# Optimization experiments

Measured on AMD Instinct MI355X. Metric: run time of the kernel, lower is better.

## Reference

```python
import jax, jax.numpy as jnp
import numpy as np

ALPHA = 0.5
BETA = 0.5


def _attend(qk, feat, W, wp, b):
    """One additive co-attention stage.
    qk:   (B, K)     projected query
    feat: (B, N, D)  keys/values
    W:    (D, K), wp: (2K, 1), b: (N,)
    returns (B, D) attention-weighted sum of feat.
    """
    proj = jnp.einsum('bnd,dk->bnk', feat, W)                    # (B,N,K)
    q = jnp.broadcast_to(qk[:, None, :], proj.shape)             # repeat query
    H = jnp.tanh(jnp.concatenate([q, proj], axis=-1))            # (B,N,2K)
    logits = jnp.einsum('bnk,k->bn', H, wp[:, 0]) + b            # (B,N)
    P = jax.nn.softmax(logits, axis=-1)
    return jnp.einsum('bn,bnd->bd', P, feat)                     # (B,D)


def setup_inputs() -> dict:
    key = jax.random.key(0)
    B, R, S, G, E, D, K = 256, 49, 128, 20, 30, 1024, 256
    ks = jax.random.split(key, 19)
    w = lambda k, shp: 0.05 * jax.random.normal(k, shp, jnp.float32)
    return {
        'ifeature_h': jax.random.normal(ks[0], (B, R, D), jnp.float32),
        'tfeature_h': jax.random.normal(ks[1], (B, S, D), jnp.float32),
        'cfeature':   jax.random.normal(ks[2], (B, G, D), jnp.float32),
        'efeature':   jax.random.normal(ks[3], (B, E, D), jnp.float32),
        'w_Vit_0':  w(ks[4],  (D, K)),
        'w_Vc_0':   w(ks[5],  (D, K)),
        'w_Pc_0':   w(ks[6],  (2 * K, 1)),
        'b_Pc_0':   jnp.zeros((G,), jnp.float32),
        'w_Ve_0':   w(ks[7],  (D, K)),
        'w_Pe_0':   w(ks[8],  (2 * K, 1)),
        'b_Pe_0':   jnp.zeros((E,), jnp.float32),
        'w_Vi_1':   w(ks[9],  (D, K)),
        'w_Vtce_1': w(ks[10], (D, K)),
        'w_Pi_1':   w(ks[11], (2 * K, 1)),
        'b_Pi_1':   jnp.zeros((R,), jnp.float32),
        'w_Vice_2': w(ks[12], (D, K)),
        'w_Vt_2':   w(ks[13], (D, K)),
        'w_Pt_2':   w(ks[14], (2 * K, 1)),
        'b_Pt_2':   jnp.zeros((S,), jnp.float32),
    }


def reference(ifeature_h, tfeature_h, cfeature, efeature,
              w_Vit_0, w_Vc_0, w_Pc_0, b_Pc_0,
              w_Ve_0, w_Pe_0, b_Pe_0,
              w_Vi_1, w_Vtce_1, w_Pi_1, b_Pi_1,
              w_Vice_2, w_Vt_2, w_Pt_2, b_Pt_2):
    ifeat = jnp.mean(ifeature_h, axis=1)   # (B, D)
    tfeat = jnp.mean(tfeature_h, axis=1)   # (B, D)

    # stage 0: image+text query attends over caption group and title
    q0 = (ifeat + tfeat) @ w_Vit_0                               # (B, K)
    Vc = _attend(q0, cfeature, w_Vc_0, w_Pc_0, b_Pc_0)           # (B, D)
    Ve = _attend(q0, efeature, w_Ve_0, w_Pe_0, b_Pe_0)           # (B, D)

    # stage 1: text+caption+title query attends over image regions
    q1 = (tfeat + ALPHA * Vc + BETA * Ve) @ w_Vtce_1
    Vi = _attend(q1, ifeature_h, w_Vi_1, w_Pi_1, b_Pi_1)

    # stage 2: image+caption+title query attends over text tokens
    q2 = (Vi + ALPHA * Vc + BETA * Ve) @ w_Vice_2
    Vt = _attend(q2, tfeature_h, w_Vt_2, w_Pt_2, b_Pt_2)

    return Vi + Vt + ALPHA * Vc + BETA * Ve
```

## Files before the change

### kernel.cpp

```cpp
#include <hip/hip_runtime.h>
#include <hip/hip_bf16.h>
#include <stdint.h>


#define D_DIM 1024
#define K_OUT 256
#define BM 64
#define BK 64
#define NT 16

typedef float f32x4 __attribute__((ext_vector_type(4)));
typedef short bf16x8 __attribute__((ext_vector_type(8)));
typedef unsigned short u16x8 __attribute__((ext_vector_type(8)));

static __device__ __forceinline__ unsigned short f2bf(float f) {
    return __builtin_bit_cast(unsigned short, __float2bfloat16(f));
}

static __device__ __forceinline__ float fast_tanh(float x) {
    float e = __expf(2.0f * x);
    return 1.0f - 2.0f / (e + 1.0f);
}

__global__ __launch_bounds__(256) void convert_wt(
    const float* __restrict__ w_c, const float* __restrict__ w_e,
    const float* __restrict__ w_i, const float* __restrict__ w_t,
    unsigned short* __restrict__ wtf)
{
    const float* wsel[4] = {w_c, w_e, w_i, w_t};
    const float* W = wsel[blockIdx.x];
    unsigned short* out = wtf + (size_t)blockIdx.x * (K_OUT * D_DIM);
    const int kb = blockIdx.y;
    const int t = threadIdx.x;

    unsigned short tmp[16];
#pragma unroll
    for (int j = 0; j < 16; ++j)
        tmp[j] = f2bf(W[(size_t)(kb * 16 + j) * K_OUT + t]);

    u16x8 lo, hi;
#pragma unroll
    for (int j = 0; j < 8; ++j) { lo[j] = tmp[j]; hi[j] = tmp[8 + j]; }
    unsigned short* dst = out + (size_t)kb * 4096 + t * 16;
    *reinterpret_cast<u16x8*>(dst) = lo;
    *reinterpret_cast<u16x8*>(dst + 8) = hi;
}

struct GemmStage {
    const float* feat;
    const unsigned short* wt;
    const float* wp;
    float* s_out;
    int blk_start;
};

__global__ __launch_bounds__(256, 3) void logits_gemm(
    GemmStage g0, GemmStage g1, GemmStage g2, GemmStage g3)
{
    __shared__ __align__(16) unsigned char As[2][BM * 128];
    __shared__ float partial[BM][4];

    const int bid = blockIdx.x;
    GemmStage st;
    if (bid < g1.blk_start) st = g0;
    else if (bid < g2.blk_start) st = g1;
    else if (bid < g3.blk_start) st = g2;
    else st = g3;
    const int m0 = (bid - st.blk_start) * BM;

    const int t = threadIdx.x;
    const int r = t >> 2, qd = t & 3;
    const int wv = t >> 6, lane = t & 63;
    const int q = lane >> 4, c16 = lane & 15;

    const float* aptr = st.feat + (size_t)(m0 + r) * D_DIM + qd * 16;
    const int wo0 = r * 128 + (((qd * 2    ) ^ (r & 7)) << 4);
    const int wo1 = r * 128 + (((qd * 2 + 1) ^ (r & 7)) << 4);
    const unsigned short* bb = st.wt + (q >> 1) * 4096
                             + ((wv * 64 + c16) << 4) + (q & 1) * 8;
    const int ck0 = ((0 * 4 + q) ^ (c16 & 7)) << 4;
    const int ck1 = ((1 * 4 + q) ^ (c16 & 7)) << 4;

    float wpf[4];
#pragma unroll
    for (int nt = 0; nt < 4; ++nt) wpf[nt] = st.wp[K_OUT + wv * 64 + nt * 16 + c16];

    f32x4 acc[4][4];
#pragma unroll
    for (int i = 0; i < 4; ++i)
#pragma unroll
        for (int j = 0; j < 4; ++j) acc[i][j] = (f32x4){0.f, 0.f, 0.f, 0.f};

    f32x4 pa[4];
#pragma unroll
    for (int j = 0; j < 4; ++j)
        pa[j] = *reinterpret_cast<const f32x4*>(aptr + j * 4);
    {
        u16x8 o0, o1;
#pragma unroll
        for (int j = 0; j < 4; ++j) {
            o0[j] = f2bf(pa[0][j]); o0[4 + j] = f2bf(pa[1][j]);
            o1[j] = f2bf(pa[2][j]); o1[4 + j] = f2bf(pa[3][j]);
        }
        *reinterpret_cast<u16x8*>(&As[0][wo0]) = o0;
        *reinterpret_cast<u16x8*>(&As[0][wo1]) = o1;
    }

#pragma unroll 1
    for (int kt = 0; kt < NT; ++kt) {
        __syncthreads();
        u16x8 bfr[2][4];
        const unsigned short* bk = bb + kt * 16384;
#pragma unroll
        for (int ks = 0; ks < 2; ++ks)
#pragma unroll
            for (int nt = 0; nt < 4; ++nt)
                bfr[ks][nt] = *reinterpret_cast<const u16x8*>(bk + ks * 8192 + nt * 256);
        const int ktn = (kt + 1) & 15;
#pragma unroll
        for (int j = 0; j < 4; ++j)
            pa[j] = *reinterpret_cast<const f32x4*>(aptr + ktn * 64 + j * 4);
        const unsigned char* buf = As[kt & 1];
#pragma unroll
        for (int ks = 0; ks < 2; ++ks) {
            const int ck = ks ? ck1 : ck0;
            bf16x8 af[4];
#pragma unroll
            for (int mt = 0; mt < 4; ++mt)
                af[mt] = *reinterpret_cast<const bf16x8*>(&buf[(mt * 16 + c16) * 128 + ck]);
#pragma unroll
            for (int mt = 0; mt < 4; ++mt)
#pragma unroll
                for (int nt = 0; nt < 4; ++nt)
                    acc[mt][nt] = __builtin_amdgcn_mfma_f32_16x16x32_bf16(
                        af[mt], __builtin_bit_cast(bf16x8, bfr[ks][nt]),
                        acc[mt][nt], 0, 0, 0);
        }
        if (kt + 1 < NT) {
            u16x8 o0, o1;
#pragma unroll
            for (int j = 0; j < 4; ++j) {
                o0[j] = f2bf(pa[0][j]); o0[4 + j] = f2bf(pa[1][j]);
                o1[j] = f2bf(pa[2][j]); o1[4 + j] = f2bf(pa[3][j]);
            }
            unsigned char* nbuf = As[(kt + 1) & 1];
            *reinterpret_cast<u16x8*>(&nbuf[wo0]) = o0;
            *reinterpret_cast<u16x8*>(&nbuf[wo1]) = o1;
        }
    }

#pragma unroll
    for (int mt = 0; mt < 4; ++mt) {
#pragma unroll
        for (int rg = 0; rg < 4; ++rg) {
            float v = 0.f;
#pragma unroll
            for (int nt = 0; nt < 4; ++nt)
                v += fast_tanh(acc[mt][nt][rg]) * wpf[nt];
            v += __shfl_xor(v, 1);
            v += __shfl_xor(v, 2);
            v += __shfl_xor(v, 4);
            v += __shfl_xor(v, 8);
            if (c16 == 0) partial[mt * 16 + q * 4 + rg][wv] = v;
        }
    }
    __syncthreads();
    if (t < BM)
        st.s_out[m0 + t] = partial[t][0] + partial[t][1] + partial[t][2] + partial[t][3];
}

struct PVStage {
    const float* s;
    const float* bias;
    const float* feat;
    float* v_out;
    int N;
};

__global__ __launch_bounds__(256) void softmax_pv(
    PVStage p0, PVStage p1, PVStage p2, PVStage p3)
{
    PVStage st = (blockIdx.y == 0) ? p0 : (blockIdx.y == 1) ? p1
               : (blockIdx.y == 2) ? p2 : p3;
    const int b = blockIdx.x, t = threadIdx.x;
    const int N = st.N;

    __shared__ float P[128];
    __shared__ float inv_s;

    if (t < N) P[t] = st.s[b * N + t] + st.bias[t];
    __syncthreads();
    if (t < 64) {
        float m = -3.4e38f;
        for (int n = t; n < N; n += 64) m = fmaxf(m, P[n]);
#pragma unroll
        for (int sh = 32; sh; sh >>= 1) m = fmaxf(m, __shfl_xor(m, sh));
        float ssum = 0.f;
        for (int n = t; n < N; n += 64) { float e = __expf(P[n] - m); P[n] = e; ssum += e; }
#pragma unroll
        for (int sh = 32; sh; sh >>= 1) ssum += __shfl_xor(ssum, sh);
        if (t == 0) inv_s = 1.0f / ssum;
    }
    __syncthreads();
    const float inv = inv_s;

    f32x4 accv = (f32x4){0.f, 0.f, 0.f, 0.f};
    const float* fb = st.feat + (size_t)b * N * D_DIM + t * 4;
    for (int n = 0; n < N; ++n) {
        f32x4 f = *reinterpret_cast<const f32x4*>(fb + (size_t)n * D_DIM);
        accv += (P[n] * inv) * f;
    }
    *reinterpret_cast<f32x4*>(&st.v_out[(size_t)b * D_DIM + t * 4]) = accv;
}

__global__ __launch_bounds__(256) void combine_out(
    const float* __restrict__ vc, const float* __restrict__ ve,
    const float* __restrict__ vi, const float* __restrict__ vt,
    float* __restrict__ out)
{
    const int i = (blockIdx.x * 256 + threadIdx.x) * 4;
    f32x4 a = *reinterpret_cast<const f32x4*>(vi + i);
    f32x4 bb = *reinterpret_cast<const f32x4*>(vt + i);
    f32x4 c = *reinterpret_cast<const f32x4*>(vc + i);
    f32x4 e = *reinterpret_cast<const f32x4*>(ve + i);
    *reinterpret_cast<f32x4*>(out + i) = a + bb + 0.5f * c + 0.5f * e;
}

extern "C" void kernel_launch(void* const* d_in, const int* in_sizes, int n_in,
                              void* d_out, int out_size, void* d_ws, size_t ws_size,
                              hipStream_t stream)
{
    const float* ifeature = (const float*)d_in[0];
    const float* tfeature = (const float*)d_in[1];
    const float* cfeature = (const float*)d_in[2];
    const float* efeature = (const float*)d_in[3];
    const float* w_Vc = (const float*)d_in[5];
    const float* w_Pc = (const float*)d_in[6];
    const float* b_Pc = (const float*)d_in[7];
    const float* w_Ve = (const float*)d_in[8];
    const float* w_Pe = (const float*)d_in[9];
    const float* b_Pe = (const float*)d_in[10];
    const float* w_Vi = (const float*)d_in[11];
    const float* w_Pi = (const float*)d_in[13];
    const float* b_Pi = (const float*)d_in[14];
    const float* w_Vt = (const float*)d_in[16];
    const float* w_Pt = (const float*)d_in[17];
    const float* b_Pt = (const float*)d_in[18];

    char* ws = (char*)d_ws;
    unsigned short* wtf = (unsigned short*)ws;
    float* s_c = (float*)(ws + 2u * 1024 * 1024);
    float* s_e = s_c + 5120;
    float* s_i = s_e + 7680;
    float* s_t = s_i + 12544;
    float* v_c = (float*)(ws + 3u * 1024 * 1024);
    float* v_e = v_c + 256 * 1024;
    float* v_i = v_e + 256 * 1024;
    float* v_t = v_i + 256 * 1024;

    convert_wt<<<dim3(4, 64), 256, 0, stream>>>(w_Vc, w_Ve, w_Vi, w_Vt, wtf);

    GemmStage g0{cfeature, wtf,          w_Pc, s_c, 0};
    GemmStage g1{efeature, wtf + 262144, w_Pe, s_e, 80};
    GemmStage g2{ifeature, wtf + 524288, w_Pi, s_i, 200};
    GemmStage g3{tfeature, wtf + 786432, w_Pt, s_t, 396};
    logits_gemm<<<908, 256, 0, stream>>>(g0, g1, g2, g3);

    PVStage p0{s_c, b_Pc, cfeature, v_c, 20};
    PVStage p1{s_e, b_Pe, efeature, v_e, 30};
    PVStage p2{s_i, b_Pi, ifeature, v_i, 49};
    PVStage p3{s_t, b_Pt, tfeature, v_t, 128};
    softmax_pv<<<dim3(256, 4), 256, 0, stream>>>(p0, p1, p2, p3);

    combine_out<<<256, 256, 0, stream>>>(v_c, v_e, v_i, v_t, (float*)d_out);
}
```

Baseline: 99.38 us.

## Use 512-thread blocks with deeper A-prefetch in logits GEMM

Doubles the logits GEMM block to 8 waves, each covering 32 output columns instead of 64, which halves per-thread accumulators and weight loads. The A-tile global loads are prefetched two k-steps ahead through two register sets in a manually unrolled loop, and each thread now converts and stores one 16-byte chunk per step. The goal is more memory-level parallelism and occupancy to hide the fp32 feature-load latency. In exchange it adds more barrier participants, and each A fragment is read from LDS by twice as many waves.

```diff
diff --git a/kernel.cpp b/kernel.cpp
--- a/kernel.cpp
+++ b/kernel.cpp
@@ -54,11 +54,11 @@
     int blk_start;
 };
 
-__global__ __launch_bounds__(256, 3) void logits_gemm(
+__global__ __launch_bounds__(512, 4) void logits_gemm(
     GemmStage g0, GemmStage g1, GemmStage g2, GemmStage g3)
 {
     __shared__ __align__(16) unsigned char As[2][BM * 128];
-    __shared__ float partial[BM][4];
+    __shared__ float partial[BM][8];
 
     const int bid = blockIdx.x;
     GemmStage st;
@@ -69,85 +69,97 @@
     const int m0 = (bid - st.blk_start) * BM;
 
     const int t = threadIdx.x;
-    const int r = t >> 2, qd = t & 3;
     const int wv = t >> 6, lane = t & 63;
     const int q = lane >> 4, c16 = lane & 15;
 
-    const float* aptr = st.feat + (size_t)(m0 + r) * D_DIM + qd * 16;
-    const int wo0 = r * 128 + (((qd * 2    ) ^ (r & 7)) << 4);
-    const int wo1 = r * 128 + (((qd * 2 + 1) ^ (r & 7)) << 4);
-    const unsigned short* bb = st.wt + (q >> 1) * 4096
-                             + ((wv * 64 + c16) << 4) + (q & 1) * 8;
-    const int ck0 = ((0 * 4 + q) ^ (c16 & 7)) << 4;
-    const int ck1 = ((1 * 4 + q) ^ (c16 & 7)) << 4;
-
-    float wpf[4];
-#pragma unroll
-    for (int nt = 0; nt < 4; ++nt) wpf[nt] = st.wp[K_OUT + wv * 64 + nt * 16 + c16];
-
-    f32x4 acc[4][4];
+    const int r = t >> 3, p = t & 7;
+    const int lc = p ^ (r & 7);
+    const float* aptr = st.feat + (size_t)(m0 + r) * D_DIM + lc * 8;
+    const int wofs = r * 128 + p * 16;
+
+    int rofs[4][2];
+#pragma unroll
+    for (int mt = 0; mt < 4; ++mt)
+#pragma unroll
+        for (int ks = 0; ks < 2; ++ks)
+            rofs[mt][ks] = (mt * 16 + c16) * 128 + ((((ks * 4 + q)) ^ (c16 & 7)) << 4);
+
+    const unsigned short* bb = st.wt + (size_t)(q >> 1) * 4096
+                             + ((wv * 32 + c16) << 4) + (q & 1) * 8;
+
+    float wpf[2];
+#pragma unroll
+    for (int nt = 0; nt < 2; ++nt) wpf[nt] = st.wp[K_OUT + wv * 32 + nt * 16 + c16];
+
+    f32x4 acc[4][2];
 #pragma unroll
     for (int i = 0; i < 4; ++i)
 #pragma unroll
-        for (int j = 0; j < 4; ++j) acc[i][j] = (f32x4){0.f, 0.f, 0.f, 0.f};
-
-    f32x4 pa[4];
-#pragma unroll
-    for (int j = 0; j < 4; ++j)
-        pa[j] = *reinterpret_cast<const f32x4*>(aptr + j * 4);
+        for (int j = 0; j < 2; ++j) acc[i][j] = (f32x4){0.f, 0.f, 0.f, 0.f};
+
+    f32x4 sa0, sa1, sb0, sb1;
+
+    sa0 = *reinterpret_cast<const f32x4*>(aptr);
+    sa1 = *reinterpret_cast<const f32x4*>(aptr + 4);
     {
-        u16x8 o0, o1;
-#pragma unroll
-        for (int j = 0; j < 4; ++j) {
-            o0[j] = f2bf(pa[0][j]); o0[4 + j] = f2bf(pa[1][j]);
-            o1[j] = f2bf(pa[2][j]); o1[4 + j] = f2bf(pa[3][j]);
-        }
-        *reinterpret_cast<u16x8*>(&As[0][wo0]) = o0;
-        *reinterpret_cast<u16x8*>(&As[0][wo1]) = o1;
+        u16x8 o;
+#pragma unroll
+        for (int j = 0; j < 4; ++j) { o[j] = f2bf(sa0[j]); o[4 + j] = f2bf(sa1[j]); }
+        *reinterpret_cast<u16x8*>(&As[0][wofs]) = o;
+    }
+    sa0 = *reinterpret_cast<const f32x4*>(aptr + 64);
+    sa1 = *reinterpret_cast<const f32x4*>(aptr + 68);
+    sb0 = *reinterpret_cast<const f32x4*>(aptr + 128);
+    sb1 = *reinterpret_cast<const f32x4*>(aptr + 132);
+    __syncthreads();
+
+#define GEMM_BODY(KT, BUFC, BUFN, S0, S1)                                      \
+    {                                                                          \
+        const int kt_ = (KT);                                                  \
+        u16x8 rb[2][2];                                                        \
+        const unsigned short* bk = bb + (size_t)kt_ * 16384;                   \
+        _Pragma("unroll")                                                      \
+        for (int ks = 0; ks < 2; ++ks)                                         \
+            _Pragma("unroll")                                                  \
+            for (int nt = 0; nt < 2; ++nt)                                     \
+                rb[ks][nt] = *reinterpret_cast<const u16x8*>(                  \
+                    bk + ks * 8192 + nt * 256);                                \
+        _Pragma("unroll")                                                      \
+        for (int ks = 0; ks < 2; ++ks) {                                       \
+            bf16x8 af[4];                                                      \
+            _Pragma("unroll")                                                  \
+            for (int mt = 0; mt < 4; ++mt)                                     \
+                af[mt] = *reinterpret_cast<const bf16x8*>(                     \
+                    &As[BUFC][rofs[mt][ks]]);                                  \
+            _Pragma("unroll")                                                  \
+            for (int mt = 0; mt < 4; ++mt)                                     \
+                _Pragma("unroll")                                              \
+                for (int nt = 0; nt < 2; ++nt)                                 \
+                    acc[mt][nt] = __builtin_amdgcn_mfma_f32_16x16x32_bf16(     \
+                        af[mt], __builtin_bit_cast(bf16x8, rb[ks][nt]),        \
+                        acc[mt][nt], 0, 0, 0);                                 \
+        }                                                                      \
+        if (kt_ + 1 < NT) {                                                    \
+            u16x8 o;                                                           \
+            _Pragma("unroll")                                                  \
+            for (int j = 0; j < 4; ++j) {                                      \
+                o[j] = f2bf(S0[j]); o[4 + j] = f2bf(S1[j]);                    \
+            }                                                                  \
+            *reinterpret_cast<u16x8*>(&As[BUFN][wofs]) = o;                    \
+            if (kt_ + 3 < NT) {                                                \
+                S0 = *reinterpret_cast<const f32x4*>(aptr + (kt_ + 3) * 64);   \
+                S1 = *reinterpret_cast<const f32x4*>(aptr + (kt_ + 3) * 64 + 4);\
+            }                                                                  \
+        }                                                                      \
+        __syncthreads();                                                       \
     }
 
 #pragma unroll 1
-    for (int kt = 0; kt < NT; ++kt) {
-        __syncthreads();
-        u16x8 bfr[2][4];
-        const unsigned short* bk = bb + kt * 16384;
-#pragma unroll
-        for (int ks = 0; ks < 2; ++ks)
-#pragma unroll
-            for (int nt = 0; nt < 4; ++nt)
-                bfr[ks][nt] = *reinterpret_cast<const u16x8*>(bk + ks * 8192 + nt * 256);
-        const int ktn = (kt + 1) & 15;
-#pragma unroll
-        for (int j = 0; j < 4; ++j)
-            pa[j] = *reinterpret_cast<const f32x4*>(aptr + ktn * 64 + j * 4);
-        const unsigned char* buf = As[kt & 1];
-#pragma unroll
-        for (int ks = 0; ks < 2; ++ks) {
-            const int ck = ks ? ck1 : ck0;
-            bf16x8 af[4];
-#pragma unroll
-            for (int mt = 0; mt < 4; ++mt)
-                af[mt] = *reinterpret_cast<const bf16x8*>(&buf[(mt * 16 + c16) * 128 + ck]);
-#pragma unroll
-            for (int mt = 0; mt < 4; ++mt)
-#pragma unroll
-                for (int nt = 0; nt < 4; ++nt)
-                    acc[mt][nt] = __builtin_amdgcn_mfma_f32_16x16x32_bf16(
-                        af[mt], __builtin_bit_cast(bf16x8, bfr[ks][nt]),
-                        acc[mt][nt], 0, 0, 0);
-        }
-        if (kt + 1 < NT) {
-            u16x8 o0, o1;
-#pragma unroll
-            for (int j = 0; j < 4; ++j) {
-                o0[j] = f2bf(pa[0][j]); o0[4 + j] = f2bf(pa[1][j]);
-                o1[j] = f2bf(pa[2][j]); o1[4 + j] = f2bf(pa[3][j]);
-            }
-            unsigned char* nbuf = As[(kt + 1) & 1];
-            *reinterpret_cast<u16x8*>(&nbuf[wo0]) = o0;
-            *reinterpret_cast<u16x8*>(&nbuf[wo1]) = o1;
-        }
-    }
+    for (int k2 = 0; k2 < NT; k2 += 2) {
+        GEMM_BODY(k2,     0, 1, sa0, sa1)
+        GEMM_BODY(k2 + 1, 1, 0, sb0, sb1)
+    }
+#undef GEMM_BODY
 
 #pragma unroll
     for (int mt = 0; mt < 4; ++mt) {
@@ -155,7 +167,7 @@
         for (int rg = 0; rg < 4; ++rg) {
             float v = 0.f;
 #pragma unroll
-            for (int nt = 0; nt < 4; ++nt)
+            for (int nt = 0; nt < 2; ++nt)
                 v += fast_tanh(acc[mt][nt][rg]) * wpf[nt];
             v += __shfl_xor(v, 1);
             v += __shfl_xor(v, 2);
@@ -165,8 +177,12 @@
         }
     }
     __syncthreads();
-    if (t < BM)
-        st.s_out[m0 + t] = partial[t][0] + partial[t][1] + partial[t][2] + partial[t][3];
+    if (t < BM) {
+        float v = 0.f;
+#pragma unroll
+        for (int w = 0; w < 8; ++w) v += partial[t][w];
+        st.s_out[m0 + t] = v;
+    }
 }
 
 struct PVStage {
@@ -264,7 +280,7 @@
     GemmStage g1{efeature, wtf + 262144, w_Pe, s_e, 80};
     GemmStage g2{ifeature, wtf + 524288, w_Pi, s_i, 200};
     GemmStage g3{tfeature, wtf + 786432, w_Pt, s_t, 396};
-    logits_gemm<<<908, 256, 0, stream>>>(g0, g1, g2, g3);
+    logits_gemm<<<908, 512, 0, stream>>>(g0, g1, g2, g3);
 
     PVStage p0{s_c, b_Pc, cfeature, v_c, 20};
     PVStage p1{s_e, b_Pe, efeature, v_e, 30};
```

New measurement: 101.9 us. +2.5%, slower.

## Enlarge logits GEMM tile to 256 rows with 16 waves per block

Applied to the files above, without the earlier changes.

The logits GEMM block grows from 64 rows and 4 waves to 256 rows and 16 waves arranged 4x4 over M and N. Each staged A tile in shared memory is now reused by four column-waves, and the grid shrinks from 908 to 227 blocks. The sync moves to the end of each iteration, and the partial reduction is rewritten to sum across the four N-waves. The cost is fewer blocks than CUs, which risks poor occupancy and load imbalance, and every wave still loads its own B fragments from global memory.

```diff
diff --git a/kernel.cpp b/kernel.cpp
--- a/kernel.cpp
+++ b/kernel.cpp
@@ -5,7 +5,7 @@
 
 #define D_DIM 1024
 #define K_OUT 256
-#define BM 64
+#define BM 256
 #define BK 64
 #define NT 16
 
@@ -54,11 +54,11 @@
     int blk_start;
 };
 
-__global__ __launch_bounds__(256, 3) void logits_gemm(
+__global__ __launch_bounds__(1024) void logits_gemm(
     GemmStage g0, GemmStage g1, GemmStage g2, GemmStage g3)
 {
     __shared__ __align__(16) unsigned char As[2][BM * 128];
-    __shared__ float partial[BM][4];
+    __shared__ float partial[BM][16];
 
     const int bid = blockIdx.x;
     GemmStage st;
@@ -69,21 +69,29 @@
     const int m0 = (bid - st.blk_start) * BM;
 
     const int t = threadIdx.x;
-    const int r = t >> 2, qd = t & 3;
     const int wv = t >> 6, lane = t & 63;
+    const int wm = wv >> 2, wn = wv & 3;
     const int q = lane >> 4, c16 = lane & 15;
 
-    const float* aptr = st.feat + (size_t)(m0 + r) * D_DIM + qd * 16;
-    const int wo0 = r * 128 + (((qd * 2    ) ^ (r & 7)) << 4);
-    const int wo1 = r * 128 + (((qd * 2 + 1) ^ (r & 7)) << 4);
-    const unsigned short* bb = st.wt + (q >> 1) * 4096
-                             + ((wv * 64 + c16) << 4) + (q & 1) * 8;
-    const int ck0 = ((0 * 4 + q) ^ (c16 & 7)) << 4;
-    const int ck1 = ((1 * 4 + q) ^ (c16 & 7)) << 4;
+    const int r = t >> 2, seg = t & 3;
+    const float* aptr = st.feat + (size_t)(m0 + r) * D_DIM + seg * 16;
+    const int wo0 = r * 128 + (((seg * 2    ) ^ (r & 7)) << 4);
+    const int wo1 = r * 128 + (((seg * 2 + 1) ^ (r & 7)) << 4);
+
+    int rofs[4][2];
+#pragma unroll
+    for (int mt = 0; mt < 4; ++mt)
+#pragma unroll
+        for (int ks = 0; ks < 2; ++ks)
+            rofs[mt][ks] = (wm * 64 + mt * 16 + c16) * 128
+                         + ((((ks * 4 + q)) ^ (c16 & 7)) << 4);
+
+    const unsigned short* bb = st.wt + (size_t)(q >> 1) * 4096
+                             + ((wn * 64 + c16) << 4) + (q & 1) * 8;
 
     float wpf[4];
 #pragma unroll
-    for (int nt = 0; nt < 4; ++nt) wpf[nt] = st.wp[K_OUT + wv * 64 + nt * 16 + c16];
+    for (int nt = 0; nt < 4; ++nt) wpf[nt] = st.wp[K_OUT + wn * 64 + nt * 16 + c16];
 
     f32x4 acc[4][4];
 #pragma unroll
@@ -91,62 +99,66 @@
 #pragma unroll
         for (int j = 0; j < 4; ++j) acc[i][j] = (f32x4){0.f, 0.f, 0.f, 0.f};
 
-    f32x4 pa[4];
-#pragma unroll
-    for (int j = 0; j < 4; ++j)
-        pa[j] = *reinterpret_cast<const f32x4*>(aptr + j * 4);
+    f32x4 pa0, pa1, pa2, pa3;
+
+    pa0 = *reinterpret_cast<const f32x4*>(aptr);
+    pa1 = *reinterpret_cast<const f32x4*>(aptr + 4);
+    pa2 = *reinterpret_cast<const f32x4*>(aptr + 8);
+    pa3 = *reinterpret_cast<const f32x4*>(aptr + 12);
     {
         u16x8 o0, o1;
 #pragma unroll
         for (int j = 0; j < 4; ++j) {
-            o0[j] = f2bf(pa[0][j]); o0[4 + j] = f2bf(pa[1][j]);
-            o1[j] = f2bf(pa[2][j]); o1[4 + j] = f2bf(pa[3][j]);
+            o0[j] = f2bf(pa0[j]); o0[4 + j] = f2bf(pa1[j]);
+            o1[j] = f2bf(pa2[j]); o1[4 + j] = f2bf(pa3[j]);
         }
         *reinterpret_cast<u16x8*>(&As[0][wo0]) = o0;
         *reinterpret_cast<u16x8*>(&As[0][wo1]) = o1;
     }
+    __syncthreads();
 
 #pragma unroll 1
     for (int kt = 0; kt < NT; ++kt) {
-        __syncthreads();
-        u16x8 bfr[2][4];
-        const unsigned short* bk = bb + kt * 16384;
-#pragma unroll
-        for (int ks = 0; ks < 2; ++ks)
+        const int cur = kt & 1;
+        if (kt + 1 < NT) {
+            const float* ap = aptr + (kt + 1) * BK;
+            pa0 = *reinterpret_cast<const f32x4*>(ap);
+            pa1 = *reinterpret_cast<const f32x4*>(ap + 4);
+            pa2 = *reinterpret_cast<const f32x4*>(ap + 8);
+            pa3 = *reinterpret_cast<const f32x4*>(ap + 12);
+        }
+        const unsigned char* buf = As[cur];
+        const unsigned short* bk = bb + (size_t)kt * 16384;
+#pragma unroll
+        for (int ks = 0; ks < 2; ++ks) {
+            u16x8 bfr[4];
 #pragma unroll
             for (int nt = 0; nt < 4; ++nt)
-                bfr[ks][nt] = *reinterpret_cast<const u16x8*>(bk + ks * 8192 + nt * 256);
-        const int ktn = (kt + 1) & 15;
-#pragma unroll
-        for (int j = 0; j < 4; ++j)
-            pa[j] = *reinterpret_cast<const f32x4*>(aptr + ktn * 64 + j * 4);
-        const unsigned char* buf = As[kt & 1];
-#pragma unroll
-        for (int ks = 0; ks < 2; ++ks) {
-            const int ck = ks ? ck1 : ck0;
+                bfr[nt] = *reinterpret_cast<const u16x8*>(bk + ks * 8192 + nt * 256);
             bf16x8 af[4];
 #pragma unroll
             for (int mt = 0; mt < 4; ++mt)
-                af[mt] = *reinterpret_cast<const bf16x8*>(&buf[(mt * 16 + c16) * 128 + ck]);
+                af[mt] = *reinterpret_cast<const bf16x8*>(&buf[rofs[mt][ks]]);
 #pragma unroll
             for (int mt = 0; mt < 4; ++mt)
 #pragma unroll
                 for (int nt = 0; nt < 4; ++nt)
                     acc[mt][nt] = __builtin_amdgcn_mfma_f32_16x16x32_bf16(
-                        af[mt], __builtin_bit_cast(bf16x8, bfr[ks][nt]),
+                        af[mt], __builtin_bit_cast(bf16x8, bfr[nt]),
                         acc[mt][nt], 0, 0, 0);
         }
         if (kt + 1 < NT) {
             u16x8 o0, o1;
 #pragma unroll
             for (int j = 0; j < 4; ++j) {
-                o0[j] = f2bf(pa[0][j]); o0[4 + j] = f2bf(pa[1][j]);
-                o1[j] = f2bf(pa[2][j]); o1[4 + j] = f2bf(pa[3][j]);
+                o0[j] = f2bf(pa0[j]); o0[4 + j] = f2bf(pa1[j]);
+                o1[j] = f2bf(pa2[j]); o1[4 + j] = f2bf(pa3[j]);
             }
-            unsigned char* nbuf = As[(kt + 1) & 1];
+            unsigned char* nbuf = As[cur ^ 1];
             *reinterpret_cast<u16x8*>(&nbuf[wo0]) = o0;
             *reinterpret_cast<u16x8*>(&nbuf[wo1]) = o1;
         }
+        __syncthreads();
     }
 
 #pragma unroll
@@ -161,12 +173,16 @@
             v += __shfl_xor(v, 2);
             v += __shfl_xor(v, 4);
             v += __shfl_xor(v, 8);
-            if (c16 == 0) partial[mt * 16 + q * 4 + rg][wv] = v;
-        }
-    }
-    __syncthreads();
-    if (t < BM)
-        st.s_out[m0 + t] = partial[t][0] + partial[t][1] + partial[t][2] + partial[t][3];
+            if (c16 == 0) partial[wm * 64 + mt * 16 + q * 4 + rg][wn * 4 + (wv & 0)] = v;
+        }
+    }
+    __syncthreads();
+    if (t < BM) {
+        float v = 0.f;
+#pragma unroll
+        for (int w = 0; w < 4; ++w) v += partial[t][w * 4];
+        st.s_out[m0 + t] = v;
+    }
 }
 
 struct PVStage {
@@ -261,10 +277,10 @@
     convert_wt<<<dim3(4, 64), 256, 0, stream>>>(w_Vc, w_Ve, w_Vi, w_Vt, wtf);
 
     GemmStage g0{cfeature, wtf,          w_Pc, s_c, 0};
-    GemmStage g1{efeature, wtf + 262144, w_Pe, s_e, 80};
-    GemmStage g2{ifeature, wtf + 524288, w_Pi, s_i, 200};
-    GemmStage g3{tfeature, wtf + 786432, w_Pt, s_t, 396};
-    logits_gemm<<<908, 256, 0, stream>>>(g0, g1, g2, g3);
+    GemmStage g1{efeature, wtf + 262144, w_Pe, s_e, 20};
+    GemmStage g2{ifeature, wtf + 524288, w_Pi, s_i, 50};
+    GemmStage g3{tfeature, wtf + 786432, w_Pt, s_t, 99};
+    logits_gemm<<<227, 1024, 0, stream>>>(g0, g1, g2, g3);
 
     PVStage p0{s_c, b_Pc, cfeature, v_c, 20};
     PVStage p1{s_e, b_Pe, efeature, v_e, 30};
```

Result: slower. 105.4 us (+6.1%).
